# Kernel tuning notes

Hardware: AMD Instinct MI355X
Metric: run time of the kernel (lower is better)

Reference implementation:

```python
import jax, jax.numpy as jnp
import numpy as np

TOPK_RADIUS = 1   # get_radius(topk=1): nearest non-self neighbor distance
TOPK_NEIGH = 10   # torch.topk(weights, 10)


def _soft_instance_loss(z_i, z_j, z_i_prob, z_j_prob, pseudo_label):
    n = z_i.shape[0]
    invalid = pseudo_label == -1
    same = pseudo_label[:, None] == pseudo_label[None, :]          # [n, n]
    same = same & (~invalid)[:, None] & (~invalid)[None, :]
    same = same & (~jnp.eye(n, dtype=bool))                        # remove diagonal
    mask = jnp.tile(same.astype(z_i_prob.dtype), (2, 2))           # [2n, 2n]

    feats = jnp.concatenate([z_i, z_j], axis=0)                    # [2n, d]
    probs = jnp.concatenate([z_i_prob, z_j_prob], axis=0)          # [2n, C]

    # ---- no_grad block of soft_neighbors_loss_L2 ----
    f = jax.lax.stop_gradient(feats)
    sq = jnp.sum(f * f, axis=1)
    d2 = sq[:, None] + sq[None, :] - 2.0 * (f @ f.T)
    pd = jnp.sqrt(jnp.maximum(d2, 0.0))                            # torch.cdist, [2n, 2n]
    b = 2 * n
    radius = jnp.sort(pd, axis=1)[:, TOPK_RADIUS][:, None]         # per-row 1-NN radius
    w = 1.0 - jnp.clip((pd - radius) / radius, 0.0, 1.0) - jnp.eye(b, dtype=pd.dtype)
    top, idx = jax.lax.top_k(w, TOPK_NEIGH)                        # [2n, 10]
    weights = jnp.zeros((b, b), pd.dtype).at[jnp.arange(b)[:, None], idx].set(top)
    weights = jax.lax.stop_gradient(weights)
    # ---- end no_grad ----

    inner = probs @ probs.T                                        # [2n, 2n]
    pull = weights * inner                                         # boosting=True -> pull only
    return jnp.mean(pull * mask)


def setup_inputs() -> dict:
    key = jax.random.key(0)
    k1, k2, k3, k4, k5 = jax.random.split(key, 5)
    n, d, C = 2048, 512, 128
    z_i = jax.random.normal(k1, (n, d), dtype=jnp.float32)
    z_j = jax.random.normal(k2, (n, d), dtype=jnp.float32)
    z_i_prob = jax.nn.softmax(jax.random.normal(k3, (n, C), dtype=jnp.float32), axis=-1)
    z_j_prob = jax.nn.softmax(jax.random.normal(k4, (n, C), dtype=jnp.float32), axis=-1)
    pseudo_label = jax.random.randint(k5, (n,), 0, C, dtype=jnp.int64 if jax.config.jax_enable_x64 else jnp.int32)
    return {"z_i": z_i, "z_j": z_j, "z_i_prob": z_i_prob, "z_j_prob": z_j_prob, "pseudo_label": pseudo_label}


def reference(z_i, z_j, z_i_prob, z_j_prob, pseudo_label):
    return _soft_instance_loss(z_i, z_j, z_i_prob, z_j_prob, pseudo_label)
```

## Files before the change

### kernel.cpp

```cpp
#include <hip/hip_runtime.h>
#include <hip/hip_bf16.h>
#include <hip/hip_fp16.h>
#include <cstdint>
#include <cstddef>

typedef __attribute__((ext_vector_type(8))) short short8;
typedef __attribute__((ext_vector_type(8))) unsigned short ushort8;
typedef __attribute__((ext_vector_type(4))) float f32x4;

#define BM 128
#define BN 128
#define BK 64
#define NSEL 10

__device__ __forceinline__ void gload_lds16(const void* g, void* l) {
  typedef const __attribute__((address_space(1))) void* gp_t;
  typedef __attribute__((address_space(3))) void* lp_t;
  __builtin_amdgcn_global_load_lds((gp_t)(unsigned long long)(uintptr_t)g,
                                   (lp_t)(unsigned int)(unsigned long long)(uintptr_t)l,
                                   16, 0, 0);
}

__device__ __forceinline__ unsigned short f2h_bits(float f) {
  __half h = __float2half(f);
  return *reinterpret_cast<unsigned short*>(&h);
}

__device__ __forceinline__ float h2f_bits(unsigned short us) {
  __half h = *reinterpret_cast<__half*>(&us);
  return __half2float(h);
}

__global__ __launch_bounds__(256)
void prep_kernel(const float* __restrict__ zi, const float* __restrict__ zj,
                 unsigned short* __restrict__ fb, float* __restrict__ sq,
                 int n, int d) {
  __shared__ float wred[4];
  const int row = blockIdx.x;
  const int t = threadIdx.x, lane = t & 63, wave = t >> 6;
  const float* src = (row < n) ? (zi + (size_t)row * d) : (zj + (size_t)(row - n) * d);
  float s = 0.f;
  for (int c = t; c < d; c += 256) {
    float v = src[c];
    s += v * v;
    __hip_bfloat16 h = __float2bfloat16(v);
    fb[(size_t)row * d + c] = *reinterpret_cast<const unsigned short*>(&h);
  }
#pragma unroll
  for (int o = 32; o; o >>= 1) s += __shfl_xor(s, o, 64);
  if (lane == 0) wred[wave] = s;
  __syncthreads();
  if (t == 0) sq[row] = ((wred[0] + wred[1]) + wred[2]) + wred[3];
}

__global__ __launch_bounds__(256)
void gemm_pd_kernel(const unsigned short* __restrict__ fb,
                    const float* __restrict__ sq,
                    __half* __restrict__ pdh, int b, int d) {
  __shared__ unsigned long long smem64[4096];
  unsigned short* smA = (unsigned short*)smem64;
  unsigned short* smB = smA + 8192;
  const int t = threadIdx.x;
  const int lane = t & 63;
  const int wave = t >> 6;
  const int wr = wave >> 1, wc = wave & 1;
  const int rowBase = blockIdx.y * BM;
  const int colBase = blockIdx.x * BN;
  const int l15 = lane & 15, l4 = lane >> 4;
  const int rsw = l15 & 7;

  f32x4 acc[4][4] = {};

  for (int kt = 0; kt < d; kt += BK) {
#pragma unroll
    for (int it = 0; it < 4; ++it) {
      const int c = it * 256 + t;
      const int r = c >> 3;
      const int us = (c & 7) ^ (r & 7);
      gload_lds16(fb + (size_t)(rowBase + r) * d + kt + us * 8, (char*)smA + c * 16);
      gload_lds16(fb + (size_t)(colBase + r) * d + kt + us * 8, (char*)smB + c * 16);
    }
    __syncthreads();
#pragma unroll
    for (int ks = 0; ks < 2; ++ks) {
      short8 af[4], bfr[4];
#pragma unroll
      for (int m = 0; m < 4; ++m)
        af[m] = *(const short8*)&smA[(wr * 64 + m * 16 + l15) * BK + (((ks * 4 + l4) ^ rsw) * 8)];
#pragma unroll
      for (int nn = 0; nn < 4; ++nn)
        bfr[nn] = *(const short8*)&smB[(wc * 64 + nn * 16 + l15) * BK + (((ks * 4 + l4) ^ rsw) * 8)];
#pragma unroll
      for (int m = 0; m < 4; ++m)
#pragma unroll
        for (int nn = 0; nn < 4; ++nn)
          acc[m][nn] = __builtin_amdgcn_mfma_f32_16x16x32_bf16(af[m], bfr[nn], acc[m][nn], 0, 0, 0);
    }
    __syncthreads();
  }

  unsigned short* tileC = (unsigned short*)smem64;
#pragma unroll
  for (int m = 0; m < 4; ++m) {
    const int r0l = wr * 64 + m * 16 + l4 * 4;
    const int gr0 = rowBase + r0l;
    const float sqr0 = sq[gr0], sqr1 = sq[gr0 + 1], sqr2 = sq[gr0 + 2], sqr3 = sq[gr0 + 3];
#pragma unroll
    for (int nn = 0; nn < 4; ++nn) {
      const int cl = wc * 64 + nn * 16 + l15;
      const int gc = colBase + cl;
      const float sqc = sq[gc];
      float d20 = fmaxf(sqr0 + sqc - 2.0f * acc[m][nn][0], 0.0f);
      float d21 = fmaxf(sqr1 + sqc - 2.0f * acc[m][nn][1], 0.0f);
      float d22 = fmaxf(sqr2 + sqc - 2.0f * acc[m][nn][2], 0.0f);
      float d23 = fmaxf(sqr3 + sqc - 2.0f * acc[m][nn][3], 0.0f);
      unsigned short b0 = (gr0 == gc) ? (unsigned short)0x7C00 : f2h_bits(d20);
      unsigned short b1 = (gr0 + 1 == gc) ? (unsigned short)0x7C00 : f2h_bits(d21);
      unsigned short b2 = (gr0 + 2 == gc) ? (unsigned short)0x7C00 : f2h_bits(d22);
      unsigned short b3 = (gr0 + 3 == gc) ? (unsigned short)0x7C00 : f2h_bits(d23);
#pragma unroll
      for (int rg = 0; rg < 4; ++rg) {
        const int rl = r0l + rg;
        const int dw = rl * 64 + (cl >> 1);
        const int phys = dw ^ (((rl >> 2) & 3) << 3);
        unsigned short bits = (rg == 0) ? b0 : (rg == 1) ? b1 : (rg == 2) ? b2 : b3;
        tileC[phys * 2 + (cl & 1)] = bits;
      }
    }
  }
  __syncthreads();

#pragma unroll
  for (int it2 = 0; it2 < 16; ++it2) {
    const int rl = it2 * 8 + (t >> 5);
    const int dwb = rl * 64 + (t & 31) * 2;
    const int phys = dwb ^ (((rl >> 2) & 3) << 3);
    const unsigned long long v = *(const unsigned long long*)((const char*)smem64 + (size_t)phys * 4);
    *(unsigned long long*)((char*)pdh + ((size_t)(rowBase + rl) * b + colBase + (t & 31) * 4) * 2) = v;
  }
}

__global__ __launch_bounds__(256)
void topk_loss_kernel(const __half* __restrict__ pdh,
                      const float* __restrict__ pi, const float* __restrict__ pj,
                      const int* __restrict__ labels,
                      float* __restrict__ rowsum,
                      int n, int C, int b) {
  const int t = threadIdx.x, lane = t & 63, wave = t >> 6;
  const int row = blockIdx.x * 4 + wave;

  const ushort8* rowp = (const ushort8*)(pdh + (size_t)row * b);
  unsigned vv[8][8];
  unsigned cmin[8];
#pragma unroll
  for (int ch = 0; ch < 8; ++ch) {
    ushort8 h = rowp[ch * 64 + lane];
    unsigned mn = 0xFFFFFFFFu;
#pragma unroll
    for (int j = 0; j < 8; ++j) {
      unsigned pk = ((unsigned)h[j] << 16) | (unsigned)(ch * 512 + lane * 8 + j);
      vv[ch][j] = pk;
      mn = min(mn, pk);
    }
    cmin[ch] = mn;
  }

  unsigned key[NSEL];
#pragma unroll
  for (int r = 0; r < NSEL; ++r) {
    unsigned best = cmin[0];
#pragma unroll
    for (int ch = 1; ch < 8; ++ch) best = min(best, cmin[ch]);
#pragma unroll
    for (int o = 32; o; o >>= 1) {
      unsigned q = __shfl_xor(best, o, 64);
      best = min(best, q);
    }
    key[r] = best;
    const int idx = (int)(best & 0xFFFFu);
    if (((idx >> 3) & 63) == lane) {
      const int ch = idx >> 9, jj = idx & 7;
#pragma unroll
      for (int cc = 0; cc < 8; ++cc) {
        if (cc == ch) {
          unsigned mn = 0xFFFFFFFFu;
#pragma unroll
          for (int j = 0; j < 8; ++j) {
            if (j == jj) vv[cc][j] = 0xFFFFFFFFu;
            mn = min(mn, vv[cc][j]);
          }
          cmin[cc] = mn;
        }
      }
    }
  }

  const float r0 = sqrtf(h2f_bits((unsigned short)(key[0] >> 16)));
  const float inv_r0 = 1.0f / r0;
  const int ri = (row < n) ? row : row - n;
  const int li = labels[ri];
  const float* pme = (row < n) ? (pi + (size_t)row * C) : (pj + (size_t)(row - n) * C);
  const float pr0 = pme[lane], pr1 = pme[lane + 64];

  float tot = 0.f;
#pragma unroll
  for (int k = 0; k < NSEL; ++k) {
    const int j = (int)(key[k] & 0xFFFFu);
    const int rj = (j < n) ? j : j - n;
    const int lj = labels[rj];
    const bool m = (li != -1) & (lj != -1) & (li == lj) & (ri != rj);
    if (m) {
      const float* q = (j < n) ? (pi + (size_t)j * C) : (pj + (size_t)(j - n) * C);
      float part = pr0 * q[lane] + pr1 * q[lane + 64];
#pragma unroll
      for (int o = 32; o; o >>= 1) part += __shfl_xor(part, o, 64);
      const float pd = sqrtf(h2f_bits((unsigned short)(key[k] >> 16)));
      const float w = 1.0f - fminf(fmaxf((pd - r0) * inv_r0, 0.0f), 1.0f);
      tot += w * part;
    }
  }
  if (lane == 0) rowsum[row] = tot;
}

__global__ __launch_bounds__(256)
void final_reduce_kernel(const float* __restrict__ rowsum, float* __restrict__ out, int b) {
  __shared__ float wredf[4];
  const int t = threadIdx.x, lane = t & 63, wave = t >> 6;
  float s = 0.f;
  for (int c = t; c < b; c += 256) s += rowsum[c];
#pragma unroll
  for (int o = 32; o; o >>= 1) s += __shfl_xor(s, o, 64);
  if (lane == 0) wredf[wave] = s;
  __syncthreads();
  if (t == 0) {
    float tot = ((wredf[0] + wredf[1]) + wredf[2]) + wredf[3];
    out[0] = tot / ((float)b * (float)b);
  }
}

extern "C" void kernel_launch(void* const* d_in, const int* in_sizes, int n_in,
                              void* d_out, int out_size, void* d_ws, size_t ws_size,
                              hipStream_t stream) {
  const float* zi = (const float*)d_in[0];
  const float* zj = (const float*)d_in[1];
  const float* pi = (const float*)d_in[2];
  const float* pj = (const float*)d_in[3];
  const int* labels = (const int*)d_in[4];

  const int n = in_sizes[4];
  const int d = in_sizes[0] / n;
  const int C = in_sizes[2] / n;
  const int b = 2 * n;

  char* ws = (char*)d_ws;
  size_t off = 0;
  unsigned short* fb = (unsigned short*)(ws + off);
  off += ((size_t)b * d * 2 + 255) & ~(size_t)255;
  float* sq = (float*)(ws + off);
  off += ((size_t)b * 4 + 255) & ~(size_t)255;
  float* rowsum = (float*)(ws + off);
  off += ((size_t)b * 4 + 255) & ~(size_t)255;
  __half* pdh = (__half*)(ws + off);
  off += (size_t)b * b * 2;
  if (ws_size < off) return;

  prep_kernel<<<b, 256, 0, stream>>>(zi, zj, fb, sq, n, d);
  dim3 grid(b / BN, b / BM);
  gemm_pd_kernel<<<grid, 256, 0, stream>>>(fb, sq, pdh, b, d);
  topk_loss_kernel<<<b / 4, 256, 0, stream>>>(pdh, pi, pj, labels, rowsum, n, C, b);
  final_reduce_kernel<<<1, 256, 0, stream>>>(rowsum, (float*)d_out, b);
}
```

Measured before the change: 55.69 us.

## Compute only upper-triangular distance tiles and write transposed copies

```diff
diff --git a/kernel.cpp b/kernel.cpp
--- a/kernel.cpp
+++ b/kernel.cpp
@@ -56,16 +56,26 @@
 __global__ __launch_bounds__(256)
 void gemm_pd_kernel(const unsigned short* __restrict__ fb,
                     const float* __restrict__ sq,
-                    __half* __restrict__ pdh, int b, int d) {
-  __shared__ unsigned long long smem64[4096];
-  unsigned short* smA = (unsigned short*)smem64;
+                    __half* __restrict__ pdh, int b, int d, int nb) {
+  __shared__ char smem[65536];
+  unsigned short* smA = (unsigned short*)smem;
   unsigned short* smB = smA + 8192;
+
   const int t = threadIdx.x;
   const int lane = t & 63;
   const int wave = t >> 6;
   const int wr = wave >> 1, wc = wave & 1;
-  const int rowBase = blockIdx.y * BM;
-  const int colBase = blockIdx.x * BN;
+
+  const int bid = blockIdx.x;
+  const int tn = 2 * nb + 1;
+  int r = (int)(((float)tn - sqrtf((float)(tn * tn) - 8.0f * (float)bid)) * 0.5f);
+  while ((r + 1) * (tn - (r + 1)) / 2 <= bid) ++r;
+  while (r * (tn - r) / 2 > bid) --r;
+  const int cidx = r + (bid - r * (tn - r) / 2);
+  const int rowBase = r * BM;
+  const int colBase = cidx * BN;
+  const bool offdiag = (r != cidx);
+
   const int l15 = lane & 15, l4 = lane >> 4;
   const int rsw = l15 & 7;
 
@@ -75,10 +85,10 @@
 #pragma unroll
     for (int it = 0; it < 4; ++it) {
       const int c = it * 256 + t;
-      const int r = c >> 3;
-      const int us = (c & 7) ^ (r & 7);
-      gload_lds16(fb + (size_t)(rowBase + r) * d + kt + us * 8, (char*)smA + c * 16);
-      gload_lds16(fb + (size_t)(colBase + r) * d + kt + us * 8, (char*)smB + c * 16);
+      const int rr = c >> 3;
+      const int us = (c & 7) ^ (rr & 7);
+      gload_lds16(fb + (size_t)(rowBase + rr) * d + kt + us * 8, (char*)smA + c * 16);
+      gload_lds16(fb + (size_t)(colBase + rr) * d + kt + us * 8, (char*)smB + c * 16);
     }
     __syncthreads();
 #pragma unroll
@@ -99,7 +109,8 @@
     __syncthreads();
   }
 
-  unsigned short* tileC = (unsigned short*)smem64;
+  unsigned short* tileC = (unsigned short*)smem;
+  unsigned short* tileT = (unsigned short*)(smem + 32768);
 #pragma unroll
   for (int m = 0; m < 4; ++m) {
     const int r0l = wr * 64 + m * 16 + l4 * 4;
@@ -126,6 +137,13 @@
         unsigned short bits = (rg == 0) ? b0 : (rg == 1) ? b1 : (rg == 2) ? b2 : b3;
         tileC[phys * 2 + (cl & 1)] = bits;
       }
+      {
+        const int dwT = cl * 64 + (r0l >> 1);
+        const int physT = dwT ^ (((cl >> 1) & 7) << 2);
+        unsigned long long v = (unsigned long long)b0 | ((unsigned long long)b1 << 16) |
+                               ((unsigned long long)b2 << 32) | ((unsigned long long)b3 << 48);
+        *(unsigned long long*)((char*)tileT + (size_t)physT * 4) = v;
+      }
     }
   }
   __syncthreads();
@@ -135,8 +153,20 @@
     const int rl = it2 * 8 + (t >> 5);
     const int dwb = rl * 64 + (t & 31) * 2;
     const int phys = dwb ^ (((rl >> 2) & 3) << 3);
-    const unsigned long long v = *(const unsigned long long*)((const char*)smem64 + (size_t)phys * 4);
+    const unsigned long long v = *(const unsigned long long*)((const char*)tileC + (size_t)phys * 4);
     *(unsigned long long*)((char*)pdh + ((size_t)(rowBase + rl) * b + colBase + (t & 31) * 4) * 2) = v;
+  }
+
+  if (offdiag) {
+#pragma unroll
+    for (int it2 = 0; it2 < 16; ++it2) {
+      const int mr = it2 * 8 + (t >> 5);
+      const int mc = (t & 31) * 4;
+      const int dwT = mr * 64 + (mc >> 1);
+      const int physT = dwT ^ (((mr >> 1) & 7) << 2);
+      const unsigned long long v = *(const unsigned long long*)((const char*)tileT + (size_t)physT * 4);
+      *(unsigned long long*)((char*)pdh + ((size_t)(colBase + mr) * b + rowBase + mc) * 2) = v;
+    }
   }
 }
 
@@ -265,8 +295,9 @@
   if (ws_size < off) return;
 
   prep_kernel<<<b, 256, 0, stream>>>(zi, zj, fb, sq, n, d);
-  dim3 grid(b / BN, b / BM);
-  gemm_pd_kernel<<<grid, 256, 0, stream>>>(fb, sq, pdh, b, d);
+  const int nb = b / BM;
+  const int ngrid = nb * (nb + 1) / 2;
+  gemm_pd_kernel<<<ngrid, 256, 0, stream>>>(fb, sq, pdh, b, d, nb);
   topk_loss_kernel<<<b / 4, 256, 0, stream>>>(pdh, pi, pj, labels, rowsum, n, C, b);
   final_reduce_kernel<<<1, 256, 0, stream>>>(rowsum, (float*)d_out, b);
 }
```

Result: no change. 56.68 us (+1.8%).

## Fuse per-tile top-k selection into distance GEMM epilogue, merge partial lists

Applied to the files above, without the earlier changes.

```diff
diff --git a/kernel.cpp b/kernel.cpp
--- a/kernel.cpp
+++ b/kernel.cpp
@@ -5,7 +5,6 @@
 #include <cstddef>
 
 typedef __attribute__((ext_vector_type(8))) short short8;
-typedef __attribute__((ext_vector_type(8))) unsigned short ushort8;
 typedef __attribute__((ext_vector_type(4))) float f32x4;
 
 #define BM 128
@@ -54,9 +53,9 @@
 }
 
 __global__ __launch_bounds__(256)
-void gemm_pd_kernel(const unsigned short* __restrict__ fb,
-                    const float* __restrict__ sq,
-                    __half* __restrict__ pdh, int b, int d) {
+void gemm_topk_kernel(const unsigned short* __restrict__ fb,
+                      const float* __restrict__ sq,
+                      unsigned* __restrict__ keysOut, int b, int d) {
   __shared__ unsigned long long smem64[4096];
   unsigned short* smA = (unsigned short*)smem64;
   unsigned short* smB = smA + 8192;
@@ -130,69 +129,102 @@
   }
   __syncthreads();
 
-#pragma unroll
-  for (int it2 = 0; it2 < 16; ++it2) {
-    const int rl = it2 * 8 + (t >> 5);
-    const int dwb = rl * 64 + (t & 31) * 2;
-    const int phys = dwb ^ (((rl >> 2) & 3) << 3);
-    const unsigned long long v = *(const unsigned long long*)((const char*)smem64 + (size_t)phys * 4);
-    *(unsigned long long*)((char*)pdh + ((size_t)(rowBase + rl) * b + colBase + (t & 31) * 4) * 2) = v;
+  const int rl = t >> 1;
+  const int half = t & 1;
+  unsigned top[NSEL];
+#pragma unroll
+  for (int k = 0; k < NSEL; ++k) top[k] = 0xFFFFFFFFu;
+#pragma unroll
+  for (int s = 0; s < 32; ++s) {
+    const int s2 = (s + rl) & 31;
+    const int dw = rl * 64 + half * 32 + s2;
+    const int phys = dw ^ (((rl >> 2) & 3) << 3);
+    const unsigned pair = *(const unsigned*)((const char*)smem64 + (size_t)phys * 4);
+    const int cl0 = half * 64 + s2 * 2;
+    const unsigned k0 = ((pair & 0xFFFFu) << 16) | (unsigned)(colBase + cl0);
+    const unsigned k1 = (pair & 0xFFFF0000u) | (unsigned)(colBase + cl0 + 1);
+    if (k0 < top[NSEL - 1]) {
+      unsigned cur = k0;
+#pragma unroll
+      for (int k = 0; k < NSEL; ++k) {
+        const unsigned lo = min(top[k], cur), hi = max(top[k], cur);
+        top[k] = lo; cur = hi;
+      }
+    }
+    if (k1 < top[NSEL - 1]) {
+      unsigned cur = k1;
+#pragma unroll
+      for (int k = 0; k < NSEL; ++k) {
+        const unsigned lo = min(top[k], cur), hi = max(top[k], cur);
+        top[k] = lo; cur = hi;
+      }
+    }
+  }
+
+  unsigned other[NSEL];
+#pragma unroll
+  for (int k = 0; k < NSEL; ++k) other[k] = __shfl_xor(top[k], 1, 64);
+#pragma unroll
+  for (int k = 0; k < NSEL; ++k) {
+    const unsigned cur0 = other[k];
+    if (cur0 < top[NSEL - 1]) {
+      unsigned cur = cur0;
+#pragma unroll
+      for (int k2 = 0; k2 < NSEL; ++k2) {
+        const unsigned lo = min(top[k2], cur), hi = max(top[k2], cur);
+        top[k2] = lo; cur = hi;
+      }
+    }
+  }
+
+  __syncthreads();
+  unsigned* lkeys = (unsigned*)smem64;
+  if (half == 0) {
+#pragma unroll
+    for (int k = 0; k < NSEL; ++k) lkeys[rl * NSEL + k] = top[k];
+  }
+  __syncthreads();
+  {
+    const size_t base = (size_t)blockIdx.x * (size_t)b * NSEL + (size_t)rowBase * NSEL;
+#pragma unroll
+    for (int i = 0; i < 5; ++i) keysOut[base + t * 5 + i] = lkeys[t * 5 + i];
   }
 }
 
 __global__ __launch_bounds__(256)
-void topk_loss_kernel(const __half* __restrict__ pdh,
-                      const float* __restrict__ pi, const float* __restrict__ pj,
-                      const int* __restrict__ labels,
-                      float* __restrict__ rowsum,
-                      int n, int C, int b) {
+void merge_loss_kernel(const unsigned* __restrict__ keys,
+                       const float* __restrict__ pi, const float* __restrict__ pj,
+                       const int* __restrict__ labels,
+                       float* __restrict__ rowsum,
+                       int n, int C, int b, int ntiles) {
   const int t = threadIdx.x, lane = t & 63, wave = t >> 6;
   const int row = blockIdx.x * 4 + wave;
-
-  const ushort8* rowp = (const ushort8*)(pdh + (size_t)row * b);
-  unsigned vv[8][8];
-  unsigned cmin[8];
-#pragma unroll
-  for (int ch = 0; ch < 8; ++ch) {
-    ushort8 h = rowp[ch * 64 + lane];
-    unsigned mn = 0xFFFFFFFFu;
-#pragma unroll
-    for (int j = 0; j < 8; ++j) {
-      unsigned pk = ((unsigned)h[j] << 16) | (unsigned)(ch * 512 + lane * 8 + j);
-      vv[ch][j] = pk;
-      mn = min(mn, pk);
-    }
-    cmin[ch] = mn;
+  const int total = ntiles * NSEL;
+
+  unsigned v[5];
+#pragma unroll
+  for (int q = 0; q < 5; ++q) {
+    const int f = q * 64 + lane;
+    if (f < total) {
+      const int tile = f / NSEL, k = f - tile * NSEL;
+      v[q] = keys[(size_t)tile * b * NSEL + (size_t)row * NSEL + k];
+    } else {
+      v[q] = 0xFFFFFFFFu;
+    }
   }
 
   unsigned key[NSEL];
 #pragma unroll
   for (int r = 0; r < NSEL; ++r) {
-    unsigned best = cmin[0];
-#pragma unroll
-    for (int ch = 1; ch < 8; ++ch) best = min(best, cmin[ch]);
+    unsigned best = min(min(min(v[0], v[1]), min(v[2], v[3])), v[4]);
 #pragma unroll
     for (int o = 32; o; o >>= 1) {
-      unsigned q = __shfl_xor(best, o, 64);
+      const unsigned q = __shfl_xor(best, o, 64);
       best = min(best, q);
     }
     key[r] = best;
-    const int idx = (int)(best & 0xFFFFu);
-    if (((idx >> 3) & 63) == lane) {
-      const int ch = idx >> 9, jj = idx & 7;
-#pragma unroll
-      for (int cc = 0; cc < 8; ++cc) {
-        if (cc == ch) {
-          unsigned mn = 0xFFFFFFFFu;
-#pragma unroll
-          for (int j = 0; j < 8; ++j) {
-            if (j == jj) vv[cc][j] = 0xFFFFFFFFu;
-            mn = min(mn, vv[cc][j]);
-          }
-          cmin[cc] = mn;
-        }
-      }
-    }
+#pragma unroll
+    for (int q = 0; q < 5; ++q) v[q] = (v[q] == best) ? 0xFFFFFFFFu : v[q];
   }
 
   const float r0 = sqrtf(h2f_bits((unsigned short)(key[0] >> 16)));
@@ -251,6 +283,7 @@
   const int d = in_sizes[0] / n;
   const int C = in_sizes[2] / n;
   const int b = 2 * n;
+  const int ntiles = b / BN;
 
   char* ws = (char*)d_ws;
   size_t off = 0;
@@ -260,13 +293,13 @@
   off += ((size_t)b * 4 + 255) & ~(size_t)255;
   float* rowsum = (float*)(ws + off);
   off += ((size_t)b * 4 + 255) & ~(size_t)255;
-  __half* pdh = (__half*)(ws + off);
-  off += (size_t)b * b * 2;
+  unsigned* keys = (unsigned*)(ws + off);
+  off += (size_t)ntiles * b * NSEL * 4;
   if (ws_size < off) return;
 
   prep_kernel<<<b, 256, 0, stream>>>(zi, zj, fb, sq, n, d);
   dim3 grid(b / BN, b / BM);
-  gemm_pd_kernel<<<grid, 256, 0, stream>>>(fb, sq, pdh, b, d);
-  topk_loss_kernel<<<b / 4, 256, 0, stream>>>(pdh, pi, pj, labels, rowsum, n, C, b);
+  gemm_topk_kernel<<<grid, 256, 0, stream>>>(fb, sq, keys, b, d);
+  merge_loss_kernel<<<b / 4, 256, 0, stream>>>(keys, pi, pj, labels, rowsum, n, C, b, ntiles);
   final_reduce_kernel<<<1, 256, 0, stream>>>(rowsum, (float*)d_out, b);
 }
```

New measurement: 66.10 us. 18.7% more time.
